# Kernel tuning notes

Measured on AMD Instinct MI355X. Metric: run time of the kernel, lower is better.

Reference implementation:

```python
import jax, jax.numpy as jnp
import numpy as np

B, L, D, H = 4, 2048, 1024, 16
HD = D // H


def setup_inputs() -> dict:
    key = jax.random.key(0)
    k1, k2, k3 = jax.random.split(key, 3)
    # xavier_uniform bounds for Linear(d, 3d) and Linear(d, d)
    b_qkv = float(np.sqrt(6.0 / (D + 3 * D)))
    b_out = float(np.sqrt(6.0 / (D + D)))
    x = jax.random.normal(k1, (B, L, D), dtype=jnp.float32)
    W_qkv = jax.random.uniform(k2, (3 * D, D), dtype=jnp.float32, minval=-b_qkv, maxval=b_qkv)
    W_out = jax.random.uniform(k3, (D, D), dtype=jnp.float32, minval=-b_out, maxval=b_out)
    return {"x": x, "W_qkv": W_qkv, "W_out": W_out}


def reference(x, W_qkv, W_out):
    b, l, d = x.shape
    # fused QKV projection: [B,L,3d] -> [3,B,H,L,Hd]
    qkv = (x @ W_qkv.T).reshape(b, l, 3, H, HD).transpose(2, 0, 3, 1, 4)
    q, k, v = qkv[0], qkv[1], qkv[2]
    # naive causal attention: full [B,H,L,L] score matrix, as in the original
    scores = jnp.einsum('bhqd,bhkd->bhqk', q, k) / (HD ** 0.5)
    mask = jnp.tril(jnp.ones((l, l), dtype=bool))  # causal mask recomputed per call
    scores = jnp.where(mask, scores, -jnp.inf)
    attn = jax.nn.softmax(scores, axis=-1)
    ctx = jnp.einsum('bhqk,bhkd->bhqd', attn, v)          # [B,H,L,Hd]
    ctx = ctx.transpose(0, 2, 1, 3).reshape(b, l, d)       # [B,L,d]
    return ctx @ W_out.T
```

## Files before the change

### kernel.cpp

```cpp
#include <hip/hip_runtime.h>

#define BB 4
#define LL 2048
#define DD 1024
#define HH 16
#define HD 64

typedef __attribute__((ext_vector_type(8))) short s16x8;
typedef __attribute__((ext_vector_type(4))) short s16x4;
typedef __attribute__((ext_vector_type(4))) float f32x4;

#define SCALE_LOG2E 0.18033688011112042f

__device__ __forceinline__ short f2bf(float f) {
  union { float f; unsigned u; } c;
  c.f = f;
  return (short)((c.u + 0x7fffu + ((c.u >> 16) & 1u)) >> 16);
}

__device__ __forceinline__ void cp16(const void* g, void* l) {
  __builtin_amdgcn_global_load_lds(
      (const __attribute__((address_space(1))) void*)g,
      (__attribute__((address_space(3))) void*)l, 16, 0, 0);
}

__global__ __launch_bounds__(256) void f2b_kernel(const float* __restrict__ in,
                                                  short* __restrict__ out, int n4) {
  int i = blockIdx.x * blockDim.x + threadIdx.x;
  if (i >= n4) return;
  float4 v = ((const float4*)in)[i];
  s16x4 o;
  o[0] = f2bf(v.x);
  o[1] = f2bf(v.y);
  o[2] = f2bf(v.z);
  o[3] = f2bf(v.w);
  ((s16x4*)out)[i] = o;
}

template <int MODE>
__global__ __launch_bounds__(256) void gemm_bt(const short* __restrict__ A,
                                               const short* __restrict__ Bm,
                                               int K, int N,
                                               short* __restrict__ qo,
                                               short* __restrict__ ko,
                                               short* __restrict__ vo,
                                               float* __restrict__ fo) {
  __shared__ __align__(16) short As[2][128 * 32];
  __shared__ __align__(16) short Bs[2][128 * 32];
  const int tid = threadIdx.x;
  const int m0 = blockIdx.y * 128, n0 = blockIdx.x * 128;
  const int wave = tid >> 6, lane = tid & 63;
  const int quad = lane >> 4, c16 = lane & 15;
  const int wr = (wave >> 1) * 64, wc = (wave & 1) * 64;

  f32x4 zero = {0.f, 0.f, 0.f, 0.f};
  f32x4 acc[4][4];
#pragma unroll
  for (int i = 0; i < 4; i++)
#pragma unroll
    for (int j = 0; j < 4; j++) acc[i][j] = zero;

  const int row1 = tid >> 2, seg = (tid & 3) * 8;
  const short* Ag = A + (size_t)(m0 + row1) * K + seg;
  const short* Bg = Bm + (size_t)(n0 + row1) * K + seg;

  auto stage = [&](int k0, int bi) {
    cp16(Ag + k0, As[bi] + wave * 512);
    cp16(Ag + (size_t)64 * K + k0, As[bi] + 2048 + wave * 512);
    cp16(Bg + k0, Bs[bi] + wave * 512);
    cp16(Bg + (size_t)64 * K + k0, Bs[bi] + 2048 + wave * 512);
  };

  stage(0, 0);
  __syncthreads();
  const int T = K >> 5;
  for (int t = 0; t < T; t++) {
    if (t + 1 < T) stage((t + 1) * 32, (t + 1) & 1);
    const short* Asb = As[t & 1];
    const short* Bsb = Bs[t & 1];
    s16x8 af[4], bf[4];
#pragma unroll
    for (int i = 0; i < 4; i++)
      af[i] = *(const s16x8*)&Asb[(wr + i * 16 + c16) * 32 + quad * 8];
#pragma unroll
    for (int j = 0; j < 4; j++)
      bf[j] = *(const s16x8*)&Bsb[(wc + j * 16 + c16) * 32 + quad * 8];
#pragma unroll
    for (int i = 0; i < 4; i++)
#pragma unroll
      for (int j = 0; j < 4; j++)
        acc[i][j] = __builtin_amdgcn_mfma_f32_16x16x32_bf16(af[i], bf[j], acc[i][j], 0, 0, 0);
    __syncthreads();
  }

  if (MODE == 0) {
#pragma unroll
    for (int j = 0; j < 4; j++) {
      const int gn = n0 + wc + j * 16 + c16;
      const int which = gn >> 10;
      const int h = (gn >> 6) & 15;
      const int hd = gn & 63;
      if (which == 2) {
#pragma unroll
        for (int i = 0; i < 4; i++)
#pragma unroll
          for (int r = 0; r < 4; r++) {
            const int gm = m0 + wr + i * 16 + quad * 4 + r;
            const int b = gm >> 11, l = gm & 2047;
            vo[((size_t)((b << 4) + h) * HD + hd) * LL + l] = f2bf(acc[i][j][r]);
          }
      } else {
        short* dst = which == 0 ? qo : ko;
        const float sc = which == 0 ? SCALE_LOG2E : 1.0f;
#pragma unroll
        for (int i = 0; i < 4; i++)
#pragma unroll
          for (int r = 0; r < 4; r++) {
            const int gm = m0 + wr + i * 16 + quad * 4 + r;
            const int b = gm >> 11, l = gm & 2047;
            dst[((size_t)((b << 4) + h) * LL + l) * HD + hd] = f2bf(acc[i][j][r] * sc);
          }
      }
    }
  } else {
#pragma unroll
    for (int i = 0; i < 4; i++)
#pragma unroll
      for (int r = 0; r < 4; r++) {
        const int gm = m0 + wr + i * 16 + quad * 4 + r;
#pragma unroll
        for (int j = 0; j < 4; j++) {
          const int gn = n0 + wc + j * 16 + c16;
          fo[(size_t)gm * N + gn] = acc[i][j][r];
        }
      }
  }
}

__global__ __launch_bounds__(256) void attn_kernel(const short* __restrict__ Qb,
                                                   const short* __restrict__ Kb,
                                                   const short* __restrict__ Vtb,
                                                   short* __restrict__ Cb) {
  const int pi = blockIdx.x;
  const int bh = blockIdx.y;
  const int tid = threadIdx.x;
  const int wave = tid >> 6, lane = tid & 63;
  const int quad = lane >> 4, c16 = lane & 15;
  const int sw = c16 & 7;
  const size_t base = (size_t)bh * LL * HD;
  const short* Q = Qb + base;
  const short* K = Kb + base;
  const short* Vt = Vtb + base;

  __shared__ __align__(16) short Ks[2][128 * 64];
  __shared__ __align__(16) short Vs[2][64 * 128];

  const f32x4 zero = {0.f, 0.f, 0.f, 0.f};
  const s16x4 ones = {(short)0x3F80, (short)0x3F80, (short)0x3F80, (short)0x3F80};

  const int k_r = lane >> 3, k_c = lane & 7;
  const int v_r = lane >> 4, v_c = lane & 15;
  auto stage = [&](int kb, int bi) {
#pragma unroll
    for (int i = 0; i < 4; i++) {
      const int gk = i * 32 + wave * 8 + k_r;
      cp16(K + (size_t)(kb + gk) * HD + ((k_c ^ (gk & 7)) * 8),
           &Ks[bi][i * 2048 + wave * 512]);
      const int gv = i * 16 + wave * 4 + v_r;
      cp16(Vt + (size_t)gv * LL + kb + ((v_c ^ (gv & 15)) * 8),
           &Vs[bi][i * 2048 + wave * 512]);
    }
  };

  auto pack4 = [&](const float* p) {
    union { float f; unsigned u; } a0, a1, a2, a3;
    a0.f = p[0]; a1.f = p[1]; a2.f = p[2]; a3.f = p[3];
    union { s16x4 v; unsigned u[2]; } r;
    r.u[0] = __builtin_amdgcn_perm(a1.u, a0.u, 0x07060302u);
    r.u[1] = __builtin_amdgcn_perm(a3.u, a2.u, 0x07060302u);
    return r.v;
  };

  for (int phase = 0; phase < 2; phase++) {
    const int qg = phase == 0 ? (15 - pi) : pi;
    const int qw = qg * 128 + wave * 32;
    const int tiles = qg + 1;

    s16x8 qf[2][2];
#pragma unroll
    for (int h = 0; h < 2; h++)
#pragma unroll
      for (int s = 0; s < 2; s++)
        qf[h][s] = *(const s16x8*)(Q + (size_t)(qw + h * 16 + c16) * HD + s * 32 + quad * 8);

    f32x4 o[2][4];
#pragma unroll
    for (int h = 0; h < 2; h++)
#pragma unroll
      for (int j = 0; j < 4; j++) o[h][j] = zero;
    f32x4 ol[2] = {zero, zero};

    stage(0, 0);
    __syncthreads();

    for (int t = 0; t < tiles; t++) {
      const int kb = t * 128;
      if (t + 1 < tiles) stage(kb + 128, (t + 1) & 1);
      const short* Kt = &Ks[t & 1][0];
      const short* Vv = &Vs[t & 1][0];

      const int D0 = qw - kb, D1 = D0 + 16;
      const int jm0 = D0 < 0 ? 0 : min((D0 >> 4) + 1, 8);
      const int jm1 = D1 < 0 ? 0 : min((D1 >> 4) + 1, 8);
      const int jb0 = D0 >> 4, jb1 = D1 >> 4;

#pragma unroll
      for (int j = 0; j < 8; j++) {
        if (j >= jm1) continue;
        s16x8 kf0 = *(const s16x8*)&Kt[(j * 16 + c16) * 64 + ((quad ^ sw) * 8)];
        s16x8 kf1 = *(const s16x8*)&Kt[(j * 16 + c16) * 64 + (((4 + quad) ^ sw) * 8)];
        s16x4 va[4];
#pragma unroll
        for (int j4 = 0; j4 < 4; j4++)
          va[j4] = *(const s16x4*)&Vv[(j4 * 16 + c16) * 128 +
                                      (((2 * j + (quad >> 1)) ^ c16) * 8) + (quad & 1) * 4];
        {
          f32x4 s = __builtin_amdgcn_mfma_f32_16x16x32_bf16(kf0, qf[1][0], zero, 0, 0, 0);
          s = __builtin_amdgcn_mfma_f32_16x16x32_bf16(kf1, qf[1][1], s, 0, 0, 0);
          float p[4];
#pragma unroll
          for (int r = 0; r < 4; r++) p[r] = exp2f(s[r]);
          if (j == jb1) {
            const int thr = c16 + D1 - j * 16 - quad * 4;
#pragma unroll
            for (int r = 0; r < 4; r++)
              if (r > thr) p[r] = 0.f;
          }
          s16x4 pb = pack4(p);
          ol[1] = __builtin_amdgcn_mfma_f32_16x16x16bf16_1k(ones, pb, ol[1], 0, 0, 0);
#pragma unroll
          for (int j4 = 0; j4 < 4; j4++)
            o[1][j4] = __builtin_amdgcn_mfma_f32_16x16x16bf16_1k(va[j4], pb, o[1][j4], 0, 0, 0);
        }
        if (j < jm0) {
          f32x4 s = __builtin_amdgcn_mfma_f32_16x16x32_bf16(kf0, qf[0][0], zero, 0, 0, 0);
          s = __builtin_amdgcn_mfma_f32_16x16x32_bf16(kf1, qf[0][1], s, 0, 0, 0);
          float p[4];
#pragma unroll
          for (int r = 0; r < 4; r++) p[r] = exp2f(s[r]);
          if (j == jb0) {
            const int thr = c16 + D0 - j * 16 - quad * 4;
#pragma unroll
            for (int r = 0; r < 4; r++)
              if (r > thr) p[r] = 0.f;
          }
          s16x4 pb = pack4(p);
          ol[0] = __builtin_amdgcn_mfma_f32_16x16x16bf16_1k(ones, pb, ol[0], 0, 0, 0);
#pragma unroll
          for (int j4 = 0; j4 < 4; j4++)
            o[0][j4] = __builtin_amdgcn_mfma_f32_16x16x16bf16_1k(va[j4], pb, o[0][j4], 0, 0, 0);
        }
      }

      __syncthreads();
    }

    const int b = bh >> 4, h2 = bh & 15;
#pragma unroll
    for (int h = 0; h < 2; h++) {
      const float inv = 1.0f / ol[h][0];
      const int q = qw + h * 16 + c16;
#pragma unroll
      for (int j4 = 0; j4 < 4; j4++) {
        s16x4 ov;
#pragma unroll
        for (int r = 0; r < 4; r++) ov[r] = f2bf(o[h][j4][r] * inv);
        *(s16x4*)&Cb[(size_t)(b * LL + q) * DD + h2 * HD + j4 * 16 + quad * 4] = ov;
      }
    }
  }
}

extern "C" void kernel_launch(void* const* d_in, const int* in_sizes, int n_in,
                              void* d_out, int out_size, void* d_ws, size_t ws_size,
                              hipStream_t stream) {
  const float* x = (const float*)d_in[0];
  const float* wqkv = (const float*)d_in[1];
  const float* wout = (const float*)d_in[2];
  float* out = (float*)d_out;

  const size_t NX = (size_t)BB * LL * DD;
  short* xb = (short*)d_ws;
  short* wqkvb = xb + NX;
  short* woutb = wqkvb + (size_t)3 * DD * DD;
  short* qb = woutb + (size_t)DD * DD;
  short* kb = qb + NX;
  short* vb = kb + NX;
  short* cb = vb + NX;

  f2b_kernel<<<dim3((unsigned)(NX / 4 / 256)), 256, 0, stream>>>(x, xb, (int)(NX / 4));
  f2b_kernel<<<dim3(3 * DD * DD / 4 / 256), 256, 0, stream>>>(wqkv, wqkvb, 3 * DD * DD / 4);
  f2b_kernel<<<dim3(DD * DD / 4 / 256), 256, 0, stream>>>(wout, woutb, DD * DD / 4);

  gemm_bt<0><<<dim3(3 * DD / 128, BB * LL / 128), 256, 0, stream>>>(
      xb, wqkvb, DD, 3 * DD, qb, kb, vb, nullptr);
  attn_kernel<<<dim3(8, BB * HH), 256, 0, stream>>>(qb, kb, vb, cb);
  gemm_bt<1><<<dim3(DD / 128, BB * LL / 128), 256, 0, stream>>>(
      cb, woutb, DD, DD, nullptr, nullptr, nullptr, out);
}
```

Baseline: 276.8 us.

## Fuse bf16 conversions, vectorize GEMM epilogue stores via swapped MFMA operands, use native exp2

Merges the three fp32-to-bf16 conversion launches into one kernel that writes contiguously into the workspace, which relies on xb, wqkvb and woutb being adjacent. In the GEMM, Q/K tiles and the output projection swap the MFMA A/B operands, so each lane holds four consecutive columns and can issue 8-byte bf16 or 16-byte fp32 vector stores instead of scalar ones. V tiles keep the original orientation so they can vector-store along L into the transposed layout. The attention softmax switches to the hardware exp2 builtin, which skips the denormal-handling wrapper.

```diff
diff --git a/kernel.cpp b/kernel.cpp
--- a/kernel.cpp
+++ b/kernel.cpp
@@ -24,11 +24,17 @@
       (__attribute__((address_space(3))) void*)l, 16, 0, 0);
 }
 
-__global__ __launch_bounds__(256) void f2b_kernel(const float* __restrict__ in,
-                                                  short* __restrict__ out, int n4) {
-  int i = blockIdx.x * blockDim.x + threadIdx.x;
-  if (i >= n4) return;
-  float4 v = ((const float4*)in)[i];
+__global__ __launch_bounds__(256) void f2b3_kernel(const float* __restrict__ x,
+                                                   const float* __restrict__ w1,
+                                                   const float* __restrict__ w2,
+                                                   short* __restrict__ out) {
+  const int i = blockIdx.x * 256 + threadIdx.x;
+  const float* src;
+  int off;
+  if (i < 2097152) { src = x; off = i; }
+  else if (i < 2883584) { src = w1; off = i - 2097152; }
+  else { src = w2; off = i - 2883584; }
+  float4 v = ((const float4*)src)[off];
   s16x4 o;
   o[0] = f2bf(v.x);
   o[1] = f2bf(v.y);
@@ -52,6 +58,7 @@
   const int wave = tid >> 6, lane = tid & 63;
   const int quad = lane >> 4, c16 = lane & 15;
   const int wr = (wave >> 1) * 64, wc = (wave & 1) * 64;
+  const bool swapped = (MODE == 1) || (n0 < 2048);
 
   f32x4 zero = {0.f, 0.f, 0.f, 0.f};
   f32x4 acc[4][4];
@@ -85,55 +92,69 @@
 #pragma unroll
     for (int j = 0; j < 4; j++)
       bf[j] = *(const s16x8*)&Bsb[(wc + j * 16 + c16) * 32 + quad * 8];
-#pragma unroll
-    for (int i = 0; i < 4; i++)
-#pragma unroll
-      for (int j = 0; j < 4; j++)
-        acc[i][j] = __builtin_amdgcn_mfma_f32_16x16x32_bf16(af[i], bf[j], acc[i][j], 0, 0, 0);
+    if (swapped) {
+#pragma unroll
+      for (int i = 0; i < 4; i++)
+#pragma unroll
+        for (int j = 0; j < 4; j++)
+          acc[i][j] = __builtin_amdgcn_mfma_f32_16x16x32_bf16(bf[j], af[i], acc[i][j], 0, 0, 0);
+    } else {
+#pragma unroll
+      for (int i = 0; i < 4; i++)
+#pragma unroll
+        for (int j = 0; j < 4; j++)
+          acc[i][j] = __builtin_amdgcn_mfma_f32_16x16x32_bf16(af[i], bf[j], acc[i][j], 0, 0, 0);
+    }
     __syncthreads();
   }
 
   if (MODE == 0) {
-#pragma unroll
-    for (int j = 0; j < 4; j++) {
-      const int gn = n0 + wc + j * 16 + c16;
-      const int which = gn >> 10;
-      const int h = (gn >> 6) & 15;
-      const int hd = gn & 63;
-      if (which == 2) {
-#pragma unroll
-        for (int i = 0; i < 4; i++)
-#pragma unroll
-          for (int r = 0; r < 4; r++) {
-            const int gm = m0 + wr + i * 16 + quad * 4 + r;
-            const int b = gm >> 11, l = gm & 2047;
-            vo[((size_t)((b << 4) + h) * HD + hd) * LL + l] = f2bf(acc[i][j][r]);
-          }
-      } else {
+    if (n0 < 2048) {
+#pragma unroll
+      for (int j = 0; j < 4; j++) {
+        const int gnb = n0 + wc + j * 16 + quad * 4;
+        const int which = gnb >> 10;
+        const int h = (gnb >> 6) & 15;
+        const int hd = gnb & 63;
         short* dst = which == 0 ? qo : ko;
         const float sc = which == 0 ? SCALE_LOG2E : 1.0f;
 #pragma unroll
-        for (int i = 0; i < 4; i++)
-#pragma unroll
-          for (int r = 0; r < 4; r++) {
-            const int gm = m0 + wr + i * 16 + quad * 4 + r;
-            const int b = gm >> 11, l = gm & 2047;
-            dst[((size_t)((b << 4) + h) * LL + l) * HD + hd] = f2bf(acc[i][j][r] * sc);
-          }
+        for (int i = 0; i < 4; i++) {
+          const int gm = m0 + wr + i * 16 + c16;
+          const int b = gm >> 11, l = gm & 2047;
+          s16x4 v;
+#pragma unroll
+          for (int r = 0; r < 4; r++) v[r] = f2bf(acc[i][j][r] * sc);
+          *(s16x4*)&dst[((size_t)((b << 4) + h) * LL + l) * HD + hd] = v;
+        }
+      }
+    } else {
+#pragma unroll
+      for (int j = 0; j < 4; j++) {
+        const int gn = n0 + wc + j * 16 + c16;
+        const int h = (gn >> 6) & 15;
+        const int hd = gn & 63;
+#pragma unroll
+        for (int i = 0; i < 4; i++) {
+          const int gmb = m0 + wr + i * 16 + quad * 4;
+          const int b = gmb >> 11, l = gmb & 2047;
+          s16x4 v;
+#pragma unroll
+          for (int r = 0; r < 4; r++) v[r] = f2bf(acc[i][j][r]);
+          *(s16x4*)&vo[((size_t)((b << 4) + h) * HD + hd) * LL + l] = v;
+        }
       }
     }
   } else {
 #pragma unroll
-    for (int i = 0; i < 4; i++)
-#pragma unroll
-      for (int r = 0; r < 4; r++) {
-        const int gm = m0 + wr + i * 16 + quad * 4 + r;
-#pragma unroll
-        for (int j = 0; j < 4; j++) {
-          const int gn = n0 + wc + j * 16 + c16;
-          fo[(size_t)gm * N + gn] = acc[i][j][r];
-        }
-      }
+    for (int i = 0; i < 4; i++) {
+      const int gm = m0 + wr + i * 16 + c16;
+#pragma unroll
+      for (int j = 0; j < 4; j++) {
+        const int gn = n0 + wc + j * 16 + quad * 4;
+        *(f32x4*)&fo[(size_t)gm * N + gn] = acc[i][j];
+      }
+    }
   }
 }
 
@@ -229,7 +250,7 @@
           s = __builtin_amdgcn_mfma_f32_16x16x32_bf16(kf1, qf[1][1], s, 0, 0, 0);
           float p[4];
 #pragma unroll
-          for (int r = 0; r < 4; r++) p[r] = exp2f(s[r]);
+          for (int r = 0; r < 4; r++) p[r] = __builtin_amdgcn_exp2f(s[r]);
           if (j == jb1) {
             const int thr = c16 + D1 - j * 16 - quad * 4;
 #pragma unroll
@@ -247,7 +268,7 @@
           s = __builtin_amdgcn_mfma_f32_16x16x32_bf16(kf1, qf[0][1], s, 0, 0, 0);
           float p[4];
 #pragma unroll
-          for (int r = 0; r < 4; r++) p[r] = exp2f(s[r]);
+          for (int r = 0; r < 4; r++) p[r] = __builtin_amdgcn_exp2f(s[r]);
           if (j == jb0) {
             const int thr = c16 + D0 - j * 16 - quad * 4;
 #pragma unroll
@@ -298,9 +319,7 @@
   short* vb = kb + NX;
   short* cb = vb + NX;
 
-  f2b_kernel<<<dim3((unsigned)(NX / 4 / 256)), 256, 0, stream>>>(x, xb, (int)(NX / 4));
-  f2b_kernel<<<dim3(3 * DD * DD / 4 / 256), 256, 0, stream>>>(wqkv, wqkvb, 3 * DD * DD / 4);
-  f2b_kernel<<<dim3(DD * DD / 4 / 256), 256, 0, stream>>>(wout, woutb, DD * DD / 4);
+  f2b3_kernel<<<dim3(12288), 256, 0, stream>>>(x, wqkv, wout, xb);
 
   gemm_bt<0><<<dim3(3 * DD / 128, BB * LL / 128), 256, 0, stream>>>(
       xb, wqkvb, DD, 3 * DD, qb, kb, vb, nullptr);
```

After: 284.0 us. 1.03x slower.
